# Optimization experiments

Hardware: AMD Instinct MI355X
Metric: run time of the kernel (lower is better)

## Reference

```python
import jax, jax.numpy as jnp
import numpy as np

B, L, D, H, NB = 64, 30, 512, 8, 6
AS, MT = 18, 4096
T = 3 * L
HD = D // H
EPS = 1e-3  # keras LayerNormalization default epsilon
CONV_FEAT = 7 * 7 * 64  # 84 ->(8,s4) 20 ->(4,s2) 9 ->(3,s1) 7


def setup_inputs() -> dict:
    key = jax.random.key(0)
    ks = iter(jax.random.split(key, 64))
    r = lambda *s: jax.random.normal(next(ks), s, jnp.float32) * 0.02
    inp = {
        'rtgs': jax.random.normal(next(ks), (B, L, 1), jnp.float32),
        'states': jax.random.uniform(next(ks), (B, L, 84, 84, 4), jnp.float32) * 255.0,
        'actions': jax.random.randint(next(ks), (B, L, 1), 0, AS),
        'timesteps': jax.random.randint(next(ks), (B, 1, 1), 0, MT + 1),
        # rtg embedding
        'W_rtg': r(1, D), 'b_rtg': r(D),
        # state conv stem (HWIO)
        'conv1_w': r(8, 8, 4, 32), 'conv1_b': r(32),
        'conv2_w': r(4, 4, 32, 64), 'conv2_b': r(64),
        'conv3_w': r(3, 3, 64, 64), 'conv3_b': r(64),
        'dense_s_w': r(CONV_FEAT, D), 'dense_s_b': r(D),
        # action embedding table
        'emb_a': r(AS, D),
        # positional embeddings
        'abs_pos': r(1, MT + 1, D), 'rel_pos': r(1, T + 1, D),
        # decoder blocks (stacked over NB)
        'ln1_g': 1.0 + r(NB, D), 'ln1_b': r(NB, D),
        'Wk': r(NB, D, D), 'bk': r(NB, D),
        'Wq': r(NB, D, D), 'bq': r(NB, D),
        'Wv': r(NB, D, D), 'bv': r(NB, D),
        'ln2_g': 1.0 + r(NB, D), 'ln2_b': r(NB, D),
        'W1': r(NB, D, 4 * D), 'b1': r(NB, 4 * D),
        'W2': r(NB, 4 * D, D), 'b2': r(NB, D),
        # final norm + head (no bias)
        'lnf_g': 1.0 + r(D), 'lnf_b': r(D),
        'W_head': r(D, AS),
    }
    return inp


def _conv(x, w, b, stride):
    y = jax.lax.conv_general_dilated(x, w, (stride, stride), 'VALID',
                                     dimension_numbers=('NHWC', 'HWIO', 'NHWC'))
    return jax.nn.relu(y + b)


def _layernorm(x, g, b):
    m = x.mean(-1, keepdims=True)
    v = ((x - m) ** 2).mean(-1, keepdims=True)
    return (x - m) / jnp.sqrt(v + EPS) * g + b


def _attn(x, Wk, bk, Wq, bq, Wv, bv):
    Bx, Tx, C = x.shape
    split = lambda z: z.reshape(Bx, Tx, H, HD).transpose(0, 2, 1, 3)  # (B,H,T,hd)
    k, q, v = split(x @ Wk + bk), split(x @ Wq + bq), split(x @ Wv + bv)
    # NOTE: faithful to source: scores = K @ Q^T (not Q @ K^T)
    s = jnp.einsum('bhid,bhjd->bhij', k, q) / jnp.sqrt(jnp.float32(HD))
    mask = jnp.tril(jnp.ones((Tx, Tx), bool))
    s = jnp.where(mask, s, -jnp.inf)
    w = jax.nn.softmax(s, axis=-1)
    o = jnp.einsum('bhij,bhjd->bhid', w, v)
    return o.transpose(0, 2, 1, 3).reshape(Bx, Tx, C)


def reference(rtgs, states, actions, timesteps, W_rtg, b_rtg,
              conv1_w, conv1_b, conv2_w, conv2_b, conv3_w, conv3_b,
              dense_s_w, dense_s_b, emb_a, abs_pos, rel_pos,
              ln1_g, ln1_b, Wk, bk, Wq, bq, Wv, bv,
              ln2_g, ln2_b, W1, b1, W2, b2, lnf_g, lnf_b, W_head):
    # embeddings
    rtg_e = jnp.tanh(rtgs @ W_rtg + b_rtg)                       # (B,L,D)
    s = states.reshape(B * L, 84, 84, 4) / 255.0
    s = _conv(s, conv1_w, conv1_b, 4)
    s = _conv(s, conv2_w, conv2_b, 2)
    s = _conv(s, conv3_w, conv3_b, 1)
    st_e = jnp.tanh(s.reshape(B, L, -1) @ dense_s_w + dense_s_b)  # (B,L,D)
    a_e = jnp.tanh(emb_a[actions[..., 0]])                        # (B,L,D)
    # positional: abs gathered at start timestep + relative
    abs_e = abs_pos[0][timesteps[:, 0, 0]][:, None, :]            # (B,1,D)
    pos = rel_pos[:, :T, :] + abs_e                               # (B,3L,D)
    # interleave (rtg, state, action) per timestep
    tokens = jnp.stack([rtg_e, st_e, a_e], axis=2).reshape(B, T, D)
    x = tokens + pos
    for i in range(NB):
        h = _layernorm(x, ln1_g[i], ln1_b[i])
        x = x + _attn(h, Wk[i], bk[i], Wq[i], bq[i], Wv[i], bv[i])
        h = _layernorm(x, ln2_g[i], ln2_b[i])
        x = x + jax.nn.gelu(h @ W1[i] + b1[i], approximate=False) @ W2[i] + b2[i]
    x = _layernorm(x, lnf_g, lnf_b)
    logits = x @ W_head                                           # (B,3L,AS)
    return logits[:, 1::3, :]                                     # state positions -> (B,L,AS)
```

## Files before the change

### kernel.cpp

```cpp
#include <hip/hip_runtime.h>
#include <hip/hip_bf16.h>

typedef __attribute__((ext_vector_type(8))) __bf16 bf16x8;
typedef __attribute__((ext_vector_type(4))) float f32x4;

#define ACT_NONE 0
#define ACT_RELU 1
#define ACT_GELU 2
#define ACT_TANH 3
#define OUT_F32 0
#define OUT_BF16 1
#define OUT_ADD 2

__device__ __forceinline__ void gll16(const void* g, void* l) {
  __builtin_amdgcn_global_load_lds(
      reinterpret_cast<const __attribute__((address_space(1))) unsigned int*>(
          reinterpret_cast<unsigned long long>(g)),
      reinterpret_cast<__attribute__((address_space(3))) unsigned int*>(
          reinterpret_cast<unsigned long long>(l)),
      16, 0, 0);
}

__device__ __forceinline__ int xcd_swz(int bid, int n) {
  const int q = n >> 3, r = n & 7, x = bid & 7, o = bid >> 3;
  return (x < r ? x * (q + 1) : r * (q + 1) + (x - r) * q) + o;
}

template<int MODE, int K>
__device__ __forceinline__ size_t a_rowbase(int m) {
  if constexpr (MODE == 0) {
    return (size_t)m * K;
  } else if constexpr (MODE == 1) {
    int img = m / 400; int p = m - img * 400; int oy = p / 20; int ox = p - oy * 20;
    return (size_t)img * 28224 + oy * 1344 + ox * 16;
  } else if constexpr (MODE == 2) {
    int img = m / 81; int p = m - img * 81; int oy = p / 9; int ox = p - oy * 9;
    return (size_t)img * 12800 + oy * 1280 + ox * 64;
  } else {
    int img = m / 49; int p = m - img * 49; int oy = p / 7; int ox = p - oy * 7;
    return (size_t)img * 5184 + oy * 576 + ox * 64;
  }
}
template<int MODE>
__device__ __forceinline__ int f_koff(int kb) {
  if constexpr (MODE == 0) return kb;
  else if constexpr (MODE == 2) return (kb >> 7) * 640 + ((kb >> 5) & 3) * 32;
  else return kb + (kb / 192) * 384;
}

__device__ __forceinline__ bf16x8 ld8f(const float* f) {
  float4 a = *(const float4*)f;
  float4 b = *(const float4*)(f + 4);
  bf16x8 r;
  r[0] = (__bf16)a.x; r[1] = (__bf16)a.y; r[2] = (__bf16)a.z; r[3] = (__bf16)a.w;
  r[4] = (__bf16)b.x; r[5] = (__bf16)b.y; r[6] = (__bf16)b.z; r[7] = (__bf16)b.w;
  return r;
}

__device__ __forceinline__ float act_apply(float v, int ACT) {
  if (ACT == ACT_RELU) return fmaxf(v, 0.f);
  if (ACT == ACT_GELU) return 0.5f * v * (1.f + erff(v * 0.70710678118f));
  if (ACT == ACT_TANH) return tanhf(v);
  return v;
}

template<int MODE, int TM, int TN, int WM, int WN, int K, int ACT, int OUTM, int LDC, int SWZ>
__global__ __launch_bounds__(256) void gemm_k(const __bf16* __restrict__ A,
                                              const __bf16* __restrict__ BT,
                                              const float* __restrict__ bias,
                                              void* __restrict__ C) {
  constexpr int SM = TM / WM, SN = TN / WN;
  constexpr int AM = SM / 16, AN = SN / 16;
  constexpr int TA = TM / 64, TB = TN / 64;
  __shared__ __align__(16) __bf16 As[TM * 32];
  __shared__ __align__(16) __bf16 Bs[TN * 32];
  const int tid = threadIdx.x;
  const int wave = tid >> 6, lane = tid & 63;
  const int quad = lane >> 4, l16 = lane & 15;
  const int wr = wave % WM, wc = wave / WM;
  const int bm = SWZ ? xcd_swz(blockIdx.x, gridDim.x) : blockIdx.x;
  const int m0 = bm * TM, n0 = blockIdx.y * TN;
  const int lrow = lane >> 2, lkc = lane & 3;

  const __bf16* ga[TA];
  const __bf16* gb[TB];
#pragma unroll
  for (int t = 0; t < TA; ++t)
    ga[t] = A + a_rowbase<MODE, K>(m0 + (wave + 4 * t) * 16 + lrow) + lkc * 8;
#pragma unroll
  for (int t = 0; t < TB; ++t)
    gb[t] = BT + (size_t)(n0 + (wave + 4 * t) * 16 + lrow) * K + lkc * 8;

  f32x4 acc[AM][AN] = {};
  for (int kt = 0; kt < K / 32; ++kt) {
    const int kb = kt * 32;
    const int fa = f_koff<MODE>(kb);
    __syncthreads();
#pragma unroll
    for (int t = 0; t < TA; ++t)
      gll16(ga[t] + fa, &As[(wave + 4 * t) * 16 * 32]);
#pragma unroll
    for (int t = 0; t < TB; ++t)
      gll16(gb[t] + kb, &Bs[(wave + 4 * t) * 16 * 32]);
    __syncthreads();
    bf16x8 af[AM], bf[AN];
#pragma unroll
    for (int mt = 0; mt < AM; ++mt)
      af[mt] = *(const bf16x8*)&As[(wr * SM + mt * 16 + l16) * 32 + quad * 8];
#pragma unroll
    for (int nt = 0; nt < AN; ++nt)
      bf[nt] = *(const bf16x8*)&Bs[(wc * SN + nt * 16 + l16) * 32 + quad * 8];
#pragma unroll
    for (int mt = 0; mt < AM; ++mt)
#pragma unroll
      for (int nt = 0; nt < AN; ++nt)
        acc[mt][nt] = __builtin_amdgcn_mfma_f32_16x16x32_bf16(af[mt], bf[nt], acc[mt][nt], 0, 0, 0);
  }

#pragma unroll
  for (int nt = 0; nt < AN; ++nt) {
    const int col = n0 + wc * SN + nt * 16 + l16;
    const float bvl = bias[col];
#pragma unroll
    for (int mt = 0; mt < AM; ++mt) {
#pragma unroll
      for (int r = 0; r < 4; ++r) {
        const int row = m0 + wr * SM + mt * 16 + quad * 4 + r;
        float v = act_apply(acc[mt][nt][r] + bvl, ACT);
        const size_t off = (size_t)row * LDC + col;
        if constexpr (OUTM == OUT_F32) ((float*)C)[off] = v;
        else if constexpr (OUTM == OUT_BF16) ((__bf16*)C)[off] = (__bf16)v;
        else ((float*)C)[off] += v;
      }
    }
  }
}

__global__ __launch_bounds__(256) void conv1_k(const float* __restrict__ A,
                                               const __bf16* __restrict__ BT,
                                               const float* __restrict__ bias,
                                               __bf16* __restrict__ C) {
  __shared__ __align__(16) __bf16 As[128 * 32];
  __shared__ __align__(16) __bf16 Bs[32 * 32];
  const int tid = threadIdx.x;
  const int wave = tid >> 6, lane = tid & 63;
  const int quad = lane >> 4, l16 = lane & 15;
  const int m0 = xcd_swz(blockIdx.x, gridDim.x) * 128;
  const int lrow = lane >> 2, lkc = lane & 3;
  const int r0 = tid >> 2, k0o = (tid & 3) * 8;
  const int r1 = r0 + 64;
  const size_t ar0 = a_rowbase<1, 256>(m0 + r0);
  const size_t ar1 = a_rowbase<1, 256>(m0 + r1);
  const __bf16* gB = BT + (size_t)(wave * 16 + lrow) * 256 + lkc * 8;

  f32x4 acc[2][2] = {};
  bf16x8 a0 = ld8f(A + ar0 + k0o);
  bf16x8 a1 = ld8f(A + ar1 + k0o);
  for (int kt = 0; kt < 8; ++kt) {
    const int kb = kt * 32;
    __syncthreads();
    if (wave < 2) gll16(gB + kb, &Bs[wave * 16 * 32]);
    *(bf16x8*)&As[r0 * 32 + k0o] = a0;
    *(bf16x8*)&As[r1 * 32 + k0o] = a1;
    __syncthreads();
    if (kt < 7) {
      const int fa = (kt + 1) * 336;
      a0 = ld8f(A + ar0 + fa + k0o);
      a1 = ld8f(A + ar1 + fa + k0o);
    }
    bf16x8 af[2], bf[2];
#pragma unroll
    for (int mt = 0; mt < 2; ++mt)
      af[mt] = *(const bf16x8*)&As[(wave * 32 + mt * 16 + l16) * 32 + quad * 8];
#pragma unroll
    for (int nt = 0; nt < 2; ++nt)
      bf[nt] = *(const bf16x8*)&Bs[(nt * 16 + l16) * 32 + quad * 8];
#pragma unroll
    for (int mt = 0; mt < 2; ++mt)
#pragma unroll
      for (int nt = 0; nt < 2; ++nt)
        acc[mt][nt] = __builtin_amdgcn_mfma_f32_16x16x32_bf16(af[mt], bf[nt], acc[mt][nt], 0, 0, 0);
  }
#pragma unroll
  for (int nt = 0; nt < 2; ++nt) {
    const int col = nt * 16 + l16;
    const float bvl = bias[col];
#pragma unroll
    for (int mt = 0; mt < 2; ++mt) {
#pragma unroll
      for (int r = 0; r < 4; ++r) {
        const int row = m0 + wave * 32 + mt * 16 + quad * 4 + r;
        C[(size_t)row * 32 + col] = (__bf16)fmaxf(acc[mt][nt][r] + bvl, 0.f);
      }
    }
  }
}

template<typename TO>
__global__ void transpose_pad(const float* __restrict__ src, TO* __restrict__ dst,
                              int R, int C, int Cpad, long long sz, long long dz, float scale) {
  src += blockIdx.z * sz; dst += blockIdx.z * dz;
  __shared__ float t[32][33];
  const int tx = threadIdx.x, ty = threadIdx.y;
  const int r0 = blockIdx.x * 32, c0 = blockIdx.y * 32;
  for (int i = ty; i < 32; i += 8) {
    int r = r0 + i, c = c0 + tx;
    t[i][tx] = (r < R && c < C) ? src[(size_t)r * C + c] : 0.f;
  }
  __syncthreads();
  for (int i = ty; i < 32; i += 8) {
    int c = c0 + i, r = r0 + tx;
    if (c < Cpad && r < R)
      dst[(size_t)c * R + r] = (c < C) ? (TO)(t[tx][i] * scale) : (TO)0.f;
  }
}

__global__ void transpose_qkv(const float* __restrict__ Wk_, const float* __restrict__ Wq_,
                              const float* __restrict__ Wv_, __bf16* __restrict__ dst) {
  const int z = blockIdx.z, which = z / 6, i = z - which * 6;
  const float* src = (which == 0 ? Wk_ : which == 1 ? Wq_ : Wv_) + (size_t)i * 512 * 512;
  __bf16* d = dst + (size_t)i * 1536 * 512 + (size_t)which * 512 * 512;
  __shared__ float t[32][33];
  const int tx = threadIdx.x, ty = threadIdx.y;
  const int r0 = blockIdx.x * 32, c0 = blockIdx.y * 32;
  for (int j = ty; j < 32; j += 8)
    t[j][tx] = src[(size_t)(r0 + j) * 512 + c0 + tx];
  __syncthreads();
  for (int j = ty; j < 32; j += 8)
    d[(size_t)(c0 + j) * 512 + r0 + tx] = (__bf16)t[tx][j];
}

__global__ void biascat_k(const float* bk, const float* bq, const float* bv, float* dst) {
  const int i = blockIdx.x;
  for (int d = threadIdx.x; d < 512; d += 256) {
    dst[i * 1536 + d] = bk[i * 512 + d];
    dst[i * 1536 + 512 + d] = bq[i * 512 + d];
    dst[i * 1536 + 1024 + d] = bv[i * 512 + d];
  }
}

__global__ void embed_k(const float* __restrict__ rtgs, const int* __restrict__ actions,
                        const int* __restrict__ timesteps, const float* __restrict__ W_rtg,
                        const float* __restrict__ b_rtg, const float* __restrict__ emb_a,
                        const float* __restrict__ abs_pos, const float* __restrict__ rel_pos,
                        const float* __restrict__ ste, float* __restrict__ x) {
  const int idx = blockIdx.x * 256 + threadIdx.x;
  const int d = idx & 511; const int rb = idx >> 9;
  const int b = rb / 90, t = rb - b * 90;
  const int l = t / 3, r = t - l * 3;
  const float pos = rel_pos[t * 512 + d] + abs_pos[(size_t)timesteps[b] * 512 + d];
  float tok;
  if (r == 0) tok = tanhf(rtgs[b * 30 + l] * W_rtg[d] + b_rtg[d]);
  else if (r == 1) tok = ste[(size_t)(b * 30 + l) * 512 + d];
  else tok = tanhf(emb_a[actions[b * 30 + l] * 512 + d]);
  x[idx] = tok + pos;
}

__global__ __launch_bounds__(256) void ln_k(const float* __restrict__ x, const float* __restrict__ g,
                                            const float* __restrict__ bb, __bf16* __restrict__ h) {
  const int row = blockIdx.x * 4 + (threadIdx.x >> 6);
  const int lane = threadIdx.x & 63;
  const float* xr = x + (size_t)row * 512;
  float4 a = *(const float4*)&xr[lane * 8];
  float4 c = *(const float4*)&xr[lane * 8 + 4];
  float vv[8] = {a.x, a.y, a.z, a.w, c.x, c.y, c.z, c.w};
  float s = 0.f, q = 0.f;
#pragma unroll
  for (int j = 0; j < 8; ++j) { s += vv[j]; q += vv[j] * vv[j]; }
  for (int o = 32; o; o >>= 1) { s += __shfl_xor(s, o); q += __shfl_xor(q, o); }
  const float mean = s * (1.f / 512.f);
  const float var = q * (1.f / 512.f) - mean * mean;
  const float rstd = rsqrtf(var + 1e-3f);
  float4 g1 = *(const float4*)&g[lane * 8];
  float4 g2 = *(const float4*)&g[lane * 8 + 4];
  float4 b1 = *(const float4*)&bb[lane * 8];
  float4 b2 = *(const float4*)&bb[lane * 8 + 4];
  float gg[8] = {g1.x, g1.y, g1.z, g1.w, g2.x, g2.y, g2.z, g2.w};
  float bbv[8] = {b1.x, b1.y, b1.z, b1.w, b2.x, b2.y, b2.z, b2.w};
  bf16x8 ov;
#pragma unroll
  for (int j = 0; j < 8; ++j)
    ov[j] = (__bf16)((vv[j] - mean) * rstd * gg[j] + bbv[j]);
  *(bf16x8*)&h[(size_t)row * 512 + lane * 8] = ov;
}

__global__ __launch_bounds__(256) void attn_k(const __bf16* __restrict__ qkv, float* __restrict__ x) {
  __shared__ __align__(16) char smem[64512];
  __bf16* kS = (__bf16*)smem;
  __bf16* qS = (__bf16*)(smem + 13824);
  __bf16* wS = (__bf16*)smem;
  float* sS = (float*)(smem + 27648);
  __bf16* vT = (__bf16*)(smem + 27648);

  const int tid = threadIdx.x;
  const int b = blockIdx.x >> 3, h = blockIdx.x & 7;
  const int wave = tid >> 6, lane = tid & 63, quad = lane >> 4, l16 = lane & 15;
  const size_t rowbase = (size_t)b * 90 * 1536 + h * 64;

  bf16x8 vreg[3];
#pragma unroll
  for (int it = 0; it < 3; ++it) {
    const int c = tid + it * 256, t = c >> 3, d8 = (c & 7) * 8;
#pragma unroll
    for (int j = 0; j < 8; ++j) vreg[it][j] = (__bf16)0.f;
    if (t < 90) vreg[it] = *(const bf16x8*)(qkv + rowbase + (size_t)t * 1536 + 1024 + d8);
  }

  for (int c = tid; c < 768; c += 256) {
    const int t = c >> 3, d8 = (c & 7) * 8;
    bf16x8 kv, qv;
#pragma unroll
    for (int j = 0; j < 8; ++j) { kv[j] = (__bf16)0.f; qv[j] = (__bf16)0.f; }
    if (t < 90) {
      const __bf16* src = qkv + rowbase + (size_t)t * 1536 + d8;
      kv = *(const bf16x8*)src;
      qv = *(const bf16x8*)(src + 512);
    }
    *(bf16x8*)&kS[t * 72 + d8] = kv;
    *(bf16x8*)&qS[t * 72 + d8] = qv;
  }
  __syncthreads();

  for (int tt = wave; tt < 36; tt += 4) {
    const int it = tt / 6, jt = tt - it * 6;
    f32x4 acc = {0.f, 0.f, 0.f, 0.f};
#pragma unroll
    for (int ks = 0; ks < 2; ++ks) {
      bf16x8 af = *(const bf16x8*)&kS[(it * 16 + l16) * 72 + ks * 32 + quad * 8];
      bf16x8 bq = *(const bf16x8*)&qS[(jt * 16 + l16) * 72 + ks * 32 + quad * 8];
      acc = __builtin_amdgcn_mfma_f32_16x16x32_bf16(af, bq, acc, 0, 0, 0);
    }
    const int col = jt * 16 + l16;
#pragma unroll
    for (int r = 0; r < 4; ++r) {
      const int row = it * 16 + quad * 4 + r;
      sS[row * 96 + col] = (col <= row && col < 90) ? acc[r] * 0.125f : -1e30f;
    }
  }
  __syncthreads();

  for (int row = wave; row < 96; row += 4) {
    const float e0 = sS[row * 96 + lane];
    const float e1 = (lane < 32) ? sS[row * 96 + 64 + lane] : -1e30f;
    float m = fmaxf(e0, e1);
    for (int o = 32; o; o >>= 1) m = fmaxf(m, __shfl_xor(m, o));
    const float p0 = __expf(e0 - m);
    const float p1 = (lane < 32) ? __expf(e1 - m) : 0.f;
    float s = p0 + p1;
    for (int o = 32; o; o >>= 1) s += __shfl_xor(s, o);
    const float inv = 1.f / s;
    wS[row * 104 + lane] = (__bf16)(p0 * inv);
    if (lane < 32) wS[row * 104 + 64 + lane] = (__bf16)(p1 * inv);
  }
  __syncthreads();

#pragma unroll
  for (int it = 0; it < 3; ++it) {
    const int c = tid + it * 256, t = c >> 3, d8 = (c & 7) * 8;
#pragma unroll
    for (int j = 0; j < 8; ++j) vT[(d8 + j) * 104 + t] = vreg[it][j];
  }
  __syncthreads();

  for (int tt = wave; tt < 24; tt += 4) {
    const int it = tt >> 2, dt = tt & 3;
    f32x4 acc = {0.f, 0.f, 0.f, 0.f};
#pragma unroll
    for (int ks = 0; ks < 3; ++ks) {
      bf16x8 aw = *(const bf16x8*)&wS[(it * 16 + l16) * 104 + ks * 32 + quad * 8];
      bf16x8 bv = *(const bf16x8*)&vT[(dt * 16 + l16) * 104 + ks * 32 + quad * 8];
      acc = __builtin_amdgcn_mfma_f32_16x16x32_bf16(aw, bv, acc, 0, 0, 0);
    }
    const int d = dt * 16 + l16;
#pragma unroll
    for (int r = 0; r < 4; ++r) {
      const int i = it * 16 + quad * 4 + r;
      if (i < 90) {
        float* p = x + (size_t)(b * 90 + i) * 512 + h * 64 + d;
        *p += acc[r];
      }
    }
  }
}

__global__ __launch_bounds__(64) void head_k(const float* __restrict__ x, const float* __restrict__ g,
                                             const float* __restrict__ bb, const float* __restrict__ whT,
                                             float* __restrict__ out) {
  const int m = blockIdx.x;
  const int b = m / 30, l = m - b * 30;
  const float* xr = x + (size_t)(b * 90 + 3 * l + 1) * 512;
  const int lane = threadIdx.x;
  float4 a = *(const float4*)&xr[lane * 8];
  float4 c = *(const float4*)&xr[lane * 8 + 4];
  float vv[8] = {a.x, a.y, a.z, a.w, c.x, c.y, c.z, c.w};
  float s = 0.f, q = 0.f;
#pragma unroll
  for (int j = 0; j < 8; ++j) { s += vv[j]; q += vv[j] * vv[j]; }
  for (int o = 32; o; o >>= 1) { s += __shfl_xor(s, o); q += __shfl_xor(q, o); }
  const float mean = s * (1.f / 512.f);
  const float var = q * (1.f / 512.f) - mean * mean;
  const float rstd = rsqrtf(var + 1e-3f);
  float4 g1 = *(const float4*)&g[lane * 8];
  float4 g2 = *(const float4*)&g[lane * 8 + 4];
  float4 b1 = *(const float4*)&bb[lane * 8];
  float4 b2 = *(const float4*)&bb[lane * 8 + 4];
  float gg[8] = {g1.x, g1.y, g1.z, g1.w, g2.x, g2.y, g2.z, g2.w};
  float bbv[8] = {b1.x, b1.y, b1.z, b1.w, b2.x, b2.y, b2.z, b2.w};
#pragma unroll
  for (int j = 0; j < 8; ++j)
    vv[j] = (vv[j] - mean) * rstd * gg[j] + bbv[j];
  for (int aa = 0; aa < 18; ++aa) {
    float4 w1v = *(const float4*)&whT[aa * 512 + lane * 8];
    float4 w2v = *(const float4*)&whT[aa * 512 + lane * 8 + 4];
    float ww[8] = {w1v.x, w1v.y, w1v.z, w1v.w, w2v.x, w2v.y, w2v.z, w2v.w};
    float d = 0.f;
#pragma unroll
    for (int j = 0; j < 8; ++j) d += vv[j] * ww[j];
    for (int o = 32; o; o >>= 1) d += __shfl_xor(d, o);
    if (lane == 0) out[m * 18 + aa] = d;
  }
}

extern "C" void kernel_launch(void* const* d_in, const int* in_sizes, int n_in,
                              void* d_out, int out_size, void* d_ws, size_t ws_size,
                              hipStream_t stream) {
  const float* rtgs = (const float*)d_in[0];
  const float* states = (const float*)d_in[1];
  const int* actions = (const int*)d_in[2];
  const int* timesteps = (const int*)d_in[3];
  const float* W_rtg = (const float*)d_in[4];
  const float* b_rtg = (const float*)d_in[5];
  const float* conv1_w = (const float*)d_in[6];
  const float* conv1_b = (const float*)d_in[7];
  const float* conv2_w = (const float*)d_in[8];
  const float* conv2_b = (const float*)d_in[9];
  const float* conv3_w = (const float*)d_in[10];
  const float* conv3_b = (const float*)d_in[11];
  const float* dense_s_w = (const float*)d_in[12];
  const float* dense_s_b = (const float*)d_in[13];
  const float* emb_a = (const float*)d_in[14];
  const float* abs_pos = (const float*)d_in[15];
  const float* rel_pos = (const float*)d_in[16];
  const float* ln1_g = (const float*)d_in[17];
  const float* ln1_b = (const float*)d_in[18];
  const float* Wk = (const float*)d_in[19];
  const float* bk = (const float*)d_in[20];
  const float* Wq = (const float*)d_in[21];
  const float* bq = (const float*)d_in[22];
  const float* Wv = (const float*)d_in[23];
  const float* bv = (const float*)d_in[24];
  const float* ln2_g = (const float*)d_in[25];
  const float* ln2_b = (const float*)d_in[26];
  const float* W1 = (const float*)d_in[27];
  const float* b1 = (const float*)d_in[28];
  const float* W2 = (const float*)d_in[29];
  const float* b2 = (const float*)d_in[30];
  const float* lnf_g = (const float*)d_in[31];
  const float* lnf_b = (const float*)d_in[32];
  const float* W_head = (const float*)d_in[33];
  float* out = (float*)d_out;

  char* W = (char*)d_ws;
  float* x = (float*)(W + 0);
  __bf16* h = (__bf16*)(W + 11796480);
  __bf16* qkvT = (__bf16*)(W + 17694720);
  __bf16* w1T = (__bf16*)(W + 27131904);
  __bf16* w2T = (__bf16*)(W + 39714816);
  __bf16* dswT = (__bf16*)(W + 52297728);
  __bf16* c1wT = (__bf16*)(W + 55508992);
  __bf16* c2wT = (__bf16*)(W + 55574528);
  __bf16* c3wT = (__bf16*)(W + 55705600);
  float* whT = (float*)(W + 55853056);
  float* bqkv = (float*)(W + 55889920);
  __bf16* c1out = (__bf16*)(W + 55926784);
  __bf16* c2out = (__bf16*)(W + 105078784);
  __bf16* c3out = (__bf16*)(W + 55926784);
  float* ste = (float*)(W + 67969024);
  __bf16* qkvb = (__bf16*)(W + 55926784);
  __bf16* mlph = (__bf16*)(W + 73621504);

  const dim3 tb(32, 8);
  transpose_pad<__bf16><<<dim3(8, 4, 1), tb, 0, stream>>>(conv1_w, c1wT, 256, 32, 128, 0, 0, 1.f / 255.f);
  transpose_pad<__bf16><<<dim3(16, 4, 1), tb, 0, stream>>>(conv2_w, c2wT, 512, 64, 128, 0, 0, 1.f);
  transpose_pad<__bf16><<<dim3(18, 4, 1), tb, 0, stream>>>(conv3_w, c3wT, 576, 64, 128, 0, 0, 1.f);
  transpose_pad<__bf16><<<dim3(98, 16, 1), tb, 0, stream>>>(dense_s_w, dswT, 3136, 512, 512, 0, 0, 1.f);
  transpose_qkv<<<dim3(16, 16, 18), tb, 0, stream>>>(Wk, Wq, Wv, qkvT);
  transpose_pad<__bf16><<<dim3(16, 64, 6), tb, 0, stream>>>(W1, w1T, 512, 2048, 2048, 512 * 2048, 2048 * 512, 1.f);
  transpose_pad<__bf16><<<dim3(64, 16, 6), tb, 0, stream>>>(W2, w2T, 2048, 512, 512, 2048 * 512, 512 * 2048, 1.f);
  transpose_pad<float><<<dim3(16, 1, 1), tb, 0, stream>>>(W_head, whT, 512, 18, 18, 0, 0, 1.f);
  biascat_k<<<6, 256, 0, stream>>>(bk, bq, bv, bqkv);

  conv1_k<<<6000, 256, 0, stream>>>(states, c1wT, conv1_b, c1out);
  gemm_k<2, 128, 64, 2, 2, 512, ACT_RELU, OUT_BF16, 64, 1><<<dim3(1215, 1), 256, 0, stream>>>(c1out, c2wT, conv2_b, c2out);
  gemm_k<3, 128, 64, 2, 2, 576, ACT_RELU, OUT_BF16, 64, 1><<<dim3(735, 1), 256, 0, stream>>>(c2out, c3wT, conv3_b, c3out);
  gemm_k<0, 64, 64, 2, 2, 3136, ACT_TANH, OUT_F32, 512, 0><<<dim3(30, 8), 256, 0, stream>>>(c3out, dswT, dense_s_b, (void*)ste);

  embed_k<<<11520, 256, 0, stream>>>(rtgs, actions, timesteps, W_rtg, b_rtg, emb_a, abs_pos, rel_pos, ste, x);

  for (int i = 0; i < 6; ++i) {
    ln_k<<<1440, 256, 0, stream>>>(x, ln1_g + i * 512, ln1_b + i * 512, h);
    gemm_k<0, 128, 128, 2, 2, 512, ACT_NONE, OUT_BF16, 1536, 0><<<dim3(45, 12), 256, 0, stream>>>(
        h, qkvT + (size_t)i * 1536 * 512, bqkv + i * 1536, qkvb);
    attn_k<<<512, 256, 0, stream>>>(qkvb, x);
    ln_k<<<1440, 256, 0, stream>>>(x, ln2_g + i * 512, ln2_b + i * 512, h);
    gemm_k<0, 128, 128, 2, 2, 512, ACT_GELU, OUT_BF16, 2048, 0><<<dim3(45, 16), 256, 0, stream>>>(
        h, w1T + (size_t)i * 2048 * 512, b1 + i * 2048, mlph);
    gemm_k<0, 64, 64, 2, 2, 2048, ACT_NONE, OUT_ADD, 512, 0><<<dim3(90, 8), 256, 0, stream>>>(
        mlph, w2T + (size_t)i * 2048 * 512, b2 + i * 512, x);
  }

  head_k<<<1920, 64, 0, stream>>>(x, lnf_g, lnf_b, whT, out);
}
```

Before: 1.373 ms.

## Double GEMM K-step to 64 with XOR-swizzled LDS layout

```diff
diff --git a/kernel.cpp b/kernel.cpp
--- a/kernel.cpp
+++ b/kernel.cpp
@@ -42,10 +42,10 @@
   }
 }
 template<int MODE>
-__device__ __forceinline__ int f_koff(int kb) {
-  if constexpr (MODE == 0) return kb;
-  else if constexpr (MODE == 2) return (kb >> 7) * 640 + ((kb >> 5) & 3) * 32;
-  else return kb + (kb / 192) * 384;
+__device__ __forceinline__ int kphys(int k) {
+  if constexpr (MODE == 0) return k;
+  else if constexpr (MODE == 2) return (k >> 7) * 640 + ((k >> 5) & 3) * 32 + (k & 31);
+  else return k + (k / 192) * 384;
 }
 
 __device__ __forceinline__ bf16x8 ld8f(const float* f) {
@@ -71,50 +71,59 @@
                                               void* __restrict__ C) {
   constexpr int SM = TM / WM, SN = TN / WN;
   constexpr int AM = SM / 16, AN = SN / 16;
-  constexpr int TA = TM / 64, TB = TN / 64;
-  __shared__ __align__(16) __bf16 As[TM * 32];
-  __shared__ __align__(16) __bf16 Bs[TN * 32];
+  constexpr int TA = TM / 32, TB = TN / 32;
+  __shared__ __align__(16) __bf16 As[TM * 64];
+  __shared__ __align__(16) __bf16 Bs[TN * 64];
   const int tid = threadIdx.x;
   const int wave = tid >> 6, lane = tid & 63;
   const int quad = lane >> 4, l16 = lane & 15;
   const int wr = wave % WM, wc = wave / WM;
   const int bm = SWZ ? xcd_swz(blockIdx.x, gridDim.x) : blockIdx.x;
   const int m0 = bm * TM, n0 = blockIdx.y * TN;
-  const int lrow = lane >> 2, lkc = lane & 3;
+  const int srow = lane >> 3;
+  const int schk = (lane & 7) ^ srow;
 
   const __bf16* ga[TA];
   const __bf16* gb[TB];
 #pragma unroll
-  for (int t = 0; t < TA; ++t)
-    ga[t] = A + a_rowbase<MODE, K>(m0 + (wave + 4 * t) * 16 + lrow) + lkc * 8;
+  for (int t = 0; t < TA; ++t) {
+    const int row = m0 + (wave + 4 * t) * 8 + srow;
+    ga[t] = A + a_rowbase<MODE, K>(row) + (MODE == 0 ? schk * 8 : 0);
+  }
 #pragma unroll
   for (int t = 0; t < TB; ++t)
-    gb[t] = BT + (size_t)(n0 + (wave + 4 * t) * 16 + lrow) * K + lkc * 8;
+    gb[t] = BT + (size_t)(n0 + (wave + 4 * t) * 8 + srow) * K + schk * 8;
 
   f32x4 acc[AM][AN] = {};
-  for (int kt = 0; kt < K / 32; ++kt) {
-    const int kb = kt * 32;
-    const int fa = f_koff<MODE>(kb);
+  for (int kt = 0; kt < K / 64; ++kt) {
+    const int kb = kt * 64;
+    int ka;
+    if constexpr (MODE == 0) ka = kb;
+    else ka = kphys<MODE>(kb + schk * 8);
     __syncthreads();
 #pragma unroll
     for (int t = 0; t < TA; ++t)
-      gll16(ga[t] + fa, &As[(wave + 4 * t) * 16 * 32]);
+      gll16(ga[t] + ka, &As[(wave + 4 * t) * 8 * 64]);
 #pragma unroll
     for (int t = 0; t < TB; ++t)
-      gll16(gb[t] + kb, &Bs[(wave + 4 * t) * 16 * 32]);
+      gll16(gb[t] + kb, &Bs[(wave + 4 * t) * 8 * 64]);
     __syncthreads();
-    bf16x8 af[AM], bf[AN];
-#pragma unroll
-    for (int mt = 0; mt < AM; ++mt)
-      af[mt] = *(const bf16x8*)&As[(wr * SM + mt * 16 + l16) * 32 + quad * 8];
-#pragma unroll
-    for (int nt = 0; nt < AN; ++nt)
-      bf[nt] = *(const bf16x8*)&Bs[(wc * SN + nt * 16 + l16) * 32 + quad * 8];
-#pragma unroll
-    for (int mt = 0; mt < AM; ++mt)
+#pragma unroll
+    for (int ks = 0; ks < 2; ++ks) {
+      const int xa = (((ks * 4 + quad) ^ (l16 & 7)) * 8);
+      bf16x8 af[AM], bq[AN];
+#pragma unroll
+      for (int mt = 0; mt < AM; ++mt)
+        af[mt] = *(const bf16x8*)&As[(wr * SM + mt * 16 + l16) * 64 + xa];
 #pragma unroll
       for (int nt = 0; nt < AN; ++nt)
-        acc[mt][nt] = __builtin_amdgcn_mfma_f32_16x16x32_bf16(af[mt], bf[nt], acc[mt][nt], 0, 0, 0);
+        bq[nt] = *(const bf16x8*)&Bs[(wc * SN + nt * 16 + l16) * 64 + xa];
+#pragma unroll
+      for (int mt = 0; mt < AM; ++mt)
+#pragma unroll
+        for (int nt = 0; nt < AN; ++nt)
+          acc[mt][nt] = __builtin_amdgcn_mfma_f32_16x16x32_bf16(af[mt], bq[nt], acc[mt][nt], 0, 0, 0);
+    }
   }
 
 #pragma unroll
```

Result: slower. 1.413 ms (+2.9%).
